# Optimization experiments

Hardware: AMD Instinct MI355X
Metric: run time of the kernel (lower is better)

Reference implementation:

```python
import jax, jax.numpy as jnp
import numpy as np

N_NODES = 50000
N_EDGES = 1600000
CHANNELS = 128
EXPANSION = 50
CUTOFF = 5.0
LOG2 = 0.6931471805599453


def shifted_softplus(x):
    return jax.nn.softplus(x) - LOG2


def gaussian_smearing(r, cutoff=CUTOFF, n=EXPANSION):
    # centers evenly spaced in [0, cutoff]; width set by spacing
    centers = jnp.linspace(0.0, cutoff, n, dtype=r.dtype)
    delta = centers[1] - centers[0]
    coef = 1.0 / (2.0 * delta * delta)
    d = r[:, None] - centers[None, :]          # [E, n]
    return jnp.exp(-coef * d * d)


def setup_inputs() -> dict:
    key = jax.random.key(0)
    ks = jax.random.split(key, 12)
    C, F = CHANNELS, EXPANSION

    def lin(k, fan_in, shape):
        bound = 1.0 / np.sqrt(fan_in)
        return jax.random.uniform(k, shape, jnp.float32, -bound, bound)

    return {
        "features": jax.random.normal(ks[0], (N_NODES, C), jnp.float32),
        "edge_distances": jax.random.uniform(ks[1], (N_EDGES,), jnp.float32) * CUTOFF,
        "W_lin": lin(ks[2], C, (C, C)),
        "Wf1": lin(ks[3], F, (F, C)), "bf1": lin(ks[4], F, (C,)),
        "Wf2": lin(ks[5], C, (C, C)), "bf2": lin(ks[6], C, (C,)),
        "Wm1": lin(ks[7], C, (C, C)), "bm1": lin(ks[8], C, (C,)),
        "Wm2": lin(ks[9], C, (C, C)), "bm2": lin(ks[10], C, (C,)),
        "senders": jax.random.randint(ks[11], (N_EDGES,), 0, N_NODES, jnp.int32),
        "receivers": jax.random.randint(jax.random.fold_in(key, 99), (N_EDGES,), 0, N_NODES, jnp.int32),
    }


def reference(features, edge_distances, W_lin, Wf1, bf1, Wf2, bf2,
              Wm1, bm1, Wm2, bm2, senders, receivers):
    # 1. linear transform of node features (no bias)
    h = features @ W_lin.T                                   # [N, C]
    # 2. learnable radial filter F(r_ij): Gaussian basis -> MLP
    basis = gaussian_smearing(edge_distances)                # [E, F]
    ef = shifted_softplus(basis @ Wf1 + bf1) @ Wf2 + bf2     # [E, C]
    # 3. gather neighbour features, elementwise multiply, scatter-sum
    messages = h[senders] * ef                               # [E, C]
    agg = jax.ops.segment_sum(messages, receivers, num_segments=N_NODES)  # [N, C]
    # 4. output MLP
    return shifted_softplus(agg @ Wm1 + bm1) @ Wm2 + bm2
```

## Files before the change

kernel.cpp:

```cpp
#include <hip/hip_runtime.h>
#include <hip/hip_bf16.h>
#include <math.h>

#define N_NODES 50000
#define N_EDGES 1600000
#define CH 128
#define NF 50
#define NR 8192
#define NB 2048
#define BUCKET_NODES 25
#define CAP 1024
#define PASSA_CHUNK 2048
#define NBLK_SCAT 782
#define NBLK_TB   128
#define NBLK_DH   782

constexpr float DELTA  = 5.0f / 49.0f;
constexpr float COEF   = 1.0f / (2.0f * DELTA * DELTA);
constexpr float LOG2_  = 0.6931471805599453f;
constexpr float RSCALE = (float)(NR - 1) / 5.0f;

typedef short  bf16x8 __attribute__((ext_vector_type(8)));
typedef float  f32x4  __attribute__((ext_vector_type(4)));
typedef unsigned short ushort_t;
typedef unsigned long long u64;

__device__ __forceinline__ float ssp(float x) {
    return fmaxf(x, 0.0f) + __logf(1.0f + __expf(-fabsf(x))) - LOG2_;
}
__device__ __forceinline__ ushort_t f2bf(float x) {
    __hip_bfloat16 b = __float2bfloat16(x);
    return *reinterpret_cast<ushort_t*>(&b);
}
__device__ __forceinline__ float bf2f(ushort_t u) {
    return __uint_as_float(((unsigned)u) << 16);
}
__device__ __forceinline__ float4 f4zero() { return make_float4(0.f, 0.f, 0.f, 0.f); }

__global__ __launch_bounds__(256) void k1_prep(const float* __restrict__ Wlin,
                                               const float* __restrict__ Wm1,
                                               const float* __restrict__ Wm2,
                                               const float* __restrict__ Wf1,
                                               const float* __restrict__ Wf2,
                                               ushort_t* __restrict__ wlhi,
                                               ushort_t* __restrict__ wllo,
                                               ushort_t* __restrict__ wm1hi,
                                               ushort_t* __restrict__ wm1lo,
                                               ushort_t* __restrict__ wm2hi,
                                               ushort_t* __restrict__ wm2lo,
                                               ushort_t* __restrict__ wf1t,
                                               ushort_t* __restrict__ wf2hi,
                                               ushort_t* __restrict__ wf2lo,
                                               int* __restrict__ bcnt) {
    const int tid = threadIdx.x;
    if (blockIdx.x == 64) {
        for (int i = tid; i < NB; i += 256) bcnt[i] = 0;
        return;
    }
    int idx = blockIdx.x * 256 + tid;
    int n = idx >> 7, k = idx & 127;
    {   float w = Wlin[(size_t)n * CH + k];
        ushort_t hi = f2bf(w); wlhi[n * CH + k] = hi; wllo[n * CH + k] = f2bf(w - bf2f(hi)); }
    {   float w = Wm1[(size_t)k * CH + n];
        ushort_t hi = f2bf(w); wm1hi[n * CH + k] = hi; wm1lo[n * CH + k] = f2bf(w - bf2f(hi)); }
    {   float w = Wm2[(size_t)k * CH + n];
        ushort_t hi = f2bf(w); wm2hi[n * CH + k] = hi; wm2lo[n * CH + k] = f2bf(w - bf2f(hi)); }
    if (k < 64) wf1t[n * 64 + k] = (k < NF) ? f2bf(Wf1[k * CH + n]) : (ushort_t)0;
    {   float w = Wf2[(size_t)k * CH + n];
        ushort_t hi = f2bf(w); wf2hi[n * CH + k] = hi; wf2lo[n * CH + k] = f2bf(w - bf2f(hi)); }
}

__device__ void scatter_body(char* smem, int blk,
                             const int* __restrict__ recv,
                             const int* __restrict__ send,
                             const float* __restrict__ dist,
                             int* __restrict__ bcnt,
                             u64* __restrict__ brec) {
    int* bcur   = (int*)smem;
    int* bbaseL = bcur + NB;
    const int tid = threadIdx.x;
    for (int i = tid; i < NB; i += 256) bcur[i] = 0;
    __syncthreads();
    const int e0 = blk * PASSA_CHUNK;
#pragma unroll
    for (int i = 0; i < 8; i++) {
        int e = e0 + tid + i * 256;
        if (e < N_EDGES) atomicAdd(&bcur[recv[e] / BUCKET_NODES], 1);
    }
    __syncthreads();
    for (int i = tid; i < NB; i += 256) {
        int c = bcur[i];
        bbaseL[i] = c ? atomicAdd(&bcnt[i], c) : 0;
        bcur[i] = 0;
    }
    __syncthreads();
#pragma unroll
    for (int i = 0; i < 8; i++) {
        int e = e0 + tid + i * 256;
        if (e < N_EDGES) {
            int r = recv[e];
            int b = r / BUCKET_NODES;
            int rank = bbaseL[b] + atomicAdd(&bcur[b], 1);
            if (rank < CAP) {
                float x = fminf(dist[e] * RSCALE, (float)(NR - 1));
                int ti = __float2int_rn(x);
                u64 rec = (u64)(unsigned)(send[e] | (r << 16)) | ((u64)ti << 32);
                brec[(size_t)b * CAP + rank] = rec;
            }
        }
    }
}

__device__ void table_body(char* smem, int blk,
                           const float* __restrict__ bf1,
                           const float* __restrict__ bf2,
                           const ushort_t* __restrict__ wf1t,
                           const ushort_t* __restrict__ wf2hi,
                           const ushort_t* __restrict__ wf2lo,
                           ushort_t* __restrict__ tabn) {
    ushort_t (*basis)[72] = (ushort_t (*)[72])smem;
    ushort_t (*t1s)[136]  = (ushort_t (*)[136])(smem + 64 * 72 * 2);
    const int tid = threadIdx.x;
    const int g0  = blk * 64;

    for (int i = tid; i < 64 * 64; i += 256) {
        int e = i >> 6, k = i & 63;
        float val = 0.f;
        if (k < NF) {
            float r = (float)(g0 + e) * (5.0f / (float)(NR - 1));
            float d = r - (float)k * DELTA;
            val = __expf(-COEF * d * d);
        }
        basis[e][k] = f2bf(val);
    }
    __syncthreads();

    const int lane = tid & 63;
    const int wv   = tid >> 6;
    const int row  = lane & 15;
    const int quad = lane >> 4;
    const int c0   = (2 * wv) * 16 + row;
    const int c1   = c0 + 16;

    f32x4 acc[2][4];
#pragma unroll
    for (int j = 0; j < 2; j++)
#pragma unroll
        for (int rt = 0; rt < 4; rt++) acc[j][rt] = (f32x4){0.f, 0.f, 0.f, 0.f};

#pragma unroll
    for (int kb = 0; kb < 64; kb += 32) {
        bf16x8 B0 = *(const bf16x8*)&wf1t[c0 * 64 + kb + quad * 8];
        bf16x8 B1 = *(const bf16x8*)&wf1t[c1 * 64 + kb + quad * 8];
#pragma unroll
        for (int rt = 0; rt < 4; rt++) {
            bf16x8 A = *(const bf16x8*)&basis[rt * 16 + row][kb + quad * 8];
            acc[0][rt] = __builtin_amdgcn_mfma_f32_16x16x32_bf16(A, B0, acc[0][rt], 0, 0, 0);
            acc[1][rt] = __builtin_amdgcn_mfma_f32_16x16x32_bf16(A, B1, acc[1][rt], 0, 0, 0);
        }
    }
    {
        float b1v[2] = { bf1[c0], bf1[c1] };
#pragma unroll
        for (int j = 0; j < 2; j++) {
            int c = j ? c1 : c0;
#pragma unroll
            for (int rt = 0; rt < 4; rt++)
#pragma unroll
                for (int rg = 0; rg < 4; rg++) {
                    int e = rt * 16 + quad * 4 + rg;
                    t1s[e][c] = f2bf(ssp(acc[j][rt][rg] + b1v[j]));
                }
        }
    }
    __syncthreads();

#pragma unroll
    for (int j = 0; j < 2; j++)
#pragma unroll
        for (int rt = 0; rt < 4; rt++) acc[j][rt] = (f32x4){0.f, 0.f, 0.f, 0.f};

#pragma unroll
    for (int kb = 0; kb < 128; kb += 32) {
        bf16x8 B0h = *(const bf16x8*)&wf2hi[c0 * CH + kb + quad * 8];
        bf16x8 B0l = *(const bf16x8*)&wf2lo[c0 * CH + kb + quad * 8];
        bf16x8 B1h = *(const bf16x8*)&wf2hi[c1 * CH + kb + quad * 8];
        bf16x8 B1l = *(const bf16x8*)&wf2lo[c1 * CH + kb + quad * 8];
#pragma unroll
        for (int rt = 0; rt < 4; rt++) {
            bf16x8 A = *(const bf16x8*)&t1s[rt * 16 + row][kb + quad * 8];
            acc[0][rt] = __builtin_amdgcn_mfma_f32_16x16x32_bf16(A, B0l, acc[0][rt], 0, 0, 0);
            acc[0][rt] = __builtin_amdgcn_mfma_f32_16x16x32_bf16(A, B0h, acc[0][rt], 0, 0, 0);
            acc[1][rt] = __builtin_amdgcn_mfma_f32_16x16x32_bf16(A, B1l, acc[1][rt], 0, 0, 0);
            acc[1][rt] = __builtin_amdgcn_mfma_f32_16x16x32_bf16(A, B1h, acc[1][rt], 0, 0, 0);
        }
    }
    {
        float b2v[2] = { bf2[c0], bf2[c1] };
#pragma unroll
        for (int j = 0; j < 2; j++) {
            int c = j ? c1 : c0;
#pragma unroll
            for (int rt = 0; rt < 4; rt++)
#pragma unroll
                for (int rg = 0; rg < 4; rg++) {
                    int g = g0 + rt * 16 + quad * 4 + rg;
                    tabn[(size_t)g * CH + c] = f2bf(acc[j][rt][rg] + b2v[j]);
                }
        }
    }
}

__device__ void dense_h_body(char* smem, int blk,
                             const float* __restrict__ X,
                             const ushort_t* __restrict__ Bhi,
                             const ushort_t* __restrict__ Blo,
                             ushort_t* __restrict__ Y) {
    ushort_t (*xs)[136] = (ushort_t (*)[136])smem;
    const int tid  = threadIdx.x;
    const int row0 = blk * 64;

#pragma unroll
    for (int i = 0; i < 8; i++) {
        int idx = tid + i * 256;
        int r   = idx >> 5;
        int c4  = (idx & 31) * 4;
        float4 v = (row0 + r < N_NODES) ? *(const float4*)&X[(size_t)(row0 + r) * CH + c4]
                                        : f4zero();
        ushort4 s;
        s.x = f2bf(v.x); s.y = f2bf(v.y); s.z = f2bf(v.z); s.w = f2bf(v.w);
        *(ushort4*)&xs[r][c4] = s;
    }
    __syncthreads();

    const int lane = tid & 63;
    const int wv   = tid >> 6;
    const int row  = lane & 15;
    const int quad = lane >> 4;
    const int c0   = (2 * wv) * 16 + row;
    const int c1   = c0 + 16;

    f32x4 acc[2][4];
#pragma unroll
    for (int j = 0; j < 2; j++)
#pragma unroll
        for (int rt = 0; rt < 4; rt++) acc[j][rt] = (f32x4){0.f, 0.f, 0.f, 0.f};

#pragma unroll
    for (int kb = 0; kb < 128; kb += 32) {
        bf16x8 B0h = *(const bf16x8*)&Bhi[(size_t)c0 * CH + kb + quad * 8];
        bf16x8 B0l = *(const bf16x8*)&Blo[(size_t)c0 * CH + kb + quad * 8];
        bf16x8 B1h = *(const bf16x8*)&Bhi[(size_t)c1 * CH + kb + quad * 8];
        bf16x8 B1l = *(const bf16x8*)&Blo[(size_t)c1 * CH + kb + quad * 8];
#pragma unroll
        for (int rt = 0; rt < 4; rt++) {
            bf16x8 A = *(const bf16x8*)&xs[rt * 16 + row][kb + quad * 8];
            acc[0][rt] = __builtin_amdgcn_mfma_f32_16x16x32_bf16(A, B0l, acc[0][rt], 0, 0, 0);
            acc[0][rt] = __builtin_amdgcn_mfma_f32_16x16x32_bf16(A, B0h, acc[0][rt], 0, 0, 0);
            acc[1][rt] = __builtin_amdgcn_mfma_f32_16x16x32_bf16(A, B1l, acc[1][rt], 0, 0, 0);
            acc[1][rt] = __builtin_amdgcn_mfma_f32_16x16x32_bf16(A, B1h, acc[1][rt], 0, 0, 0);
        }
    }

#pragma unroll
    for (int j = 0; j < 2; j++) {
        int c = j ? c1 : c0;
#pragma unroll
        for (int rt = 0; rt < 4; rt++)
#pragma unroll
            for (int rg = 0; rg < 4; rg++) {
                int r = row0 + rt * 16 + quad * 4 + rg;
                if (r < N_NODES) Y[(size_t)r * CH + c] = f2bf(acc[j][rt][rg]);
            }
    }
}

__global__ __launch_bounds__(256) void k2_mega(const int* __restrict__ recv,
                                               const int* __restrict__ send,
                                               const float* __restrict__ dist,
                                               int* __restrict__ bcnt,
                                               u64* __restrict__ brec,
                                               const float* __restrict__ bf1,
                                               const float* __restrict__ bf2,
                                               const ushort_t* __restrict__ wf1t,
                                               const ushort_t* __restrict__ wf2hi,
                                               const ushort_t* __restrict__ wf2lo,
                                               ushort_t* __restrict__ tabn,
                                               const float* __restrict__ X,
                                               const ushort_t* __restrict__ wlhi,
                                               const ushort_t* __restrict__ wllo,
                                               ushort_t* __restrict__ h) {
    __shared__ __align__(16) char smem[64 * 72 * 2 + 64 * 136 * 2];
    const int blk = blockIdx.x;
    if (blk < 2 * NBLK_SCAT) {
        if (blk & 1) scatter_body(smem, blk >> 1, recv, send, dist, bcnt, brec);
        else         dense_h_body(smem, blk >> 1, X, wlhi, wllo, h);
    } else {
        table_body(smem, blk - 2 * NBLK_SCAT, bf1, bf2, wf1t, wf2hi, wf2lo, tabn);
    }
}

__global__ __launch_bounds__(256) void sort_gather_mlp(const int* __restrict__ bcnt,
                                                       const u64* __restrict__ brec,
                                                       const ushort_t* __restrict__ h,
                                                       const ushort_t* __restrict__ tabn,
                                                       const ushort_t* __restrict__ B1hi,
                                                       const ushort_t* __restrict__ B1lo,
                                                       const float* __restrict__ bm1,
                                                       const ushort_t* __restrict__ B2hi,
                                                       const ushort_t* __restrict__ B2lo,
                                                       const float* __restrict__ bm2,
                                                       float* __restrict__ OUT) {
    __shared__ int shist[BUCKET_NODES];
    __shared__ int sbeg[BUCKET_NODES];
    __shared__ int sexc[BUCKET_NODES];
    __shared__ unsigned sout[CAP];
    __shared__ __align__(16) ushort_t at[32][136];
    const int b = blockIdx.x, tid = threadIdx.x;
    const int nbase = b * BUCKET_NODES;
    const int nn = min(BUCKET_NODES, N_NODES - nbase);
    if (nn <= 0) return;
    const int m = min(bcnt[b], CAP);
    const u64* my = brec + (size_t)b * CAP;

    for (int i = tid; i < nn; i += 256) shist[i] = 0;
    for (int i = tid; i < 32 * 17; i += 256) {
        bf16x8 z = (bf16x8){0, 0, 0, 0, 0, 0, 0, 0};
        *(bf16x8*)&at[i / 17][(i % 17) * 8] = z;
    }
    __syncthreads();
    for (int i = tid; i < m; i += 256) {
        u64 rec = my[i];
        int l = (int)((rec >> 16) & 0xFFFF) - nbase;
        atomicAdd(&shist[l], 1);
    }
    __syncthreads();
    if (tid == 0) {
        int acc = 0;
#pragma unroll
        for (int l = 0; l < BUCKET_NODES; l++) {
            if (l < nn) { sexc[l] = acc; sbeg[l] = acc; acc += shist[l]; }
        }
    }
    __syncthreads();
    for (int i = tid; i < m; i += 256) {
        u64 rec = my[i];
        int l = (int)((rec >> 16) & 0xFFFF) - nbase;
        int rank = atomicAdd(&sexc[l], 1);
        sout[rank] = (unsigned)(rec & 0xFFFF) | ((unsigned)((rec >> 32) & 0x3FFF) << 16);
    }
    __syncthreads();

    {
        const int g  = tid >> 4;
        const int c8 = (tid & 15) * 8;
        for (int l = g; l < nn; l += 16) {
            const int beg = sbeg[l], end = sbeg[l] + shist[l];
            float acc[8];
#pragma unroll
            for (int j = 0; j < 8; j++) acc[j] = 0.f;

            int e = beg;
            for (; e + 8 <= end; e += 8) {
                unsigned v[8];
#pragma unroll
                for (int u = 0; u < 8; u++) v[u] = sout[e + u];
                bf16x8 hu[8], tn[8];
#pragma unroll
                for (int u = 0; u < 8; u++) {
                    int s  = (int)(v[u] & 0xFFFF);
                    int ti = (int)(v[u] >> 16);
                    hu[u] = *(const bf16x8*)&h[(size_t)s * CH + c8];
                    tn[u] = *(const bf16x8*)&tabn[(size_t)ti * CH + c8];
                }
#pragma unroll
                for (int u = 0; u < 8; u++)
#pragma unroll
                    for (int j = 0; j < 8; j++)
                        acc[j] = fmaf(bf2f((ushort_t)hu[u][j]), bf2f((ushort_t)tn[u][j]), acc[j]);
            }
            for (; e + 4 <= end; e += 4) {
                unsigned v[4];
#pragma unroll
                for (int u = 0; u < 4; u++) v[u] = sout[e + u];
                bf16x8 hu[4], tn[4];
#pragma unroll
                for (int u = 0; u < 4; u++) {
                    int s  = (int)(v[u] & 0xFFFF);
                    int ti = (int)(v[u] >> 16);
                    hu[u] = *(const bf16x8*)&h[(size_t)s * CH + c8];
                    tn[u] = *(const bf16x8*)&tabn[(size_t)ti * CH + c8];
                }
#pragma unroll
                for (int u = 0; u < 4; u++)
#pragma unroll
                    for (int j = 0; j < 8; j++)
                        acc[j] = fmaf(bf2f((ushort_t)hu[u][j]), bf2f((ushort_t)tn[u][j]), acc[j]);
            }
            for (; e < end; e++) {
                unsigned v = sout[e];
                int s  = (int)(v & 0xFFFF);
                int ti = (int)(v >> 16);
                bf16x8 hu = *(const bf16x8*)&h[(size_t)s * CH + c8];
                bf16x8 tn = *(const bf16x8*)&tabn[(size_t)ti * CH + c8];
#pragma unroll
                for (int j = 0; j < 8; j++)
                    acc[j] = fmaf(bf2f((ushort_t)hu[j]), bf2f((ushort_t)tn[j]), acc[j]);
            }

            bf16x8 o;
#pragma unroll
            for (int j = 0; j < 8; j++) o[j] = (short)f2bf(acc[j]);
            *(bf16x8*)&at[l][c8] = o;
        }
    }
    __syncthreads();

    const int lane = tid & 63;
    const int wv   = tid >> 6;
    const int row  = lane & 15;
    const int quad = lane >> 4;
    const int c0   = (2 * wv) * 16 + row;
    const int c1   = c0 + 16;

    f32x4 acc[2][2];
#pragma unroll
    for (int j = 0; j < 2; j++)
#pragma unroll
        for (int rt = 0; rt < 2; rt++) acc[j][rt] = (f32x4){0.f, 0.f, 0.f, 0.f};

#pragma unroll
    for (int kb = 0; kb < 128; kb += 32) {
        bf16x8 B0h = *(const bf16x8*)&B1hi[(size_t)c0 * CH + kb + quad * 8];
        bf16x8 B0l = *(const bf16x8*)&B1lo[(size_t)c0 * CH + kb + quad * 8];
        bf16x8 B1h_ = *(const bf16x8*)&B1hi[(size_t)c1 * CH + kb + quad * 8];
        bf16x8 B1l_ = *(const bf16x8*)&B1lo[(size_t)c1 * CH + kb + quad * 8];
#pragma unroll
        for (int rt = 0; rt < 2; rt++) {
            bf16x8 A = *(const bf16x8*)&at[rt * 16 + row][kb + quad * 8];
            acc[0][rt] = __builtin_amdgcn_mfma_f32_16x16x32_bf16(A, B0l, acc[0][rt], 0, 0, 0);
            acc[0][rt] = __builtin_amdgcn_mfma_f32_16x16x32_bf16(A, B0h, acc[0][rt], 0, 0, 0);
            acc[1][rt] = __builtin_amdgcn_mfma_f32_16x16x32_bf16(A, B1l_, acc[1][rt], 0, 0, 0);
            acc[1][rt] = __builtin_amdgcn_mfma_f32_16x16x32_bf16(A, B1h_, acc[1][rt], 0, 0, 0);
        }
    }
    __syncthreads();
    {
        float bv[2] = { bm1[c0], bm1[c1] };
#pragma unroll
        for (int j = 0; j < 2; j++) {
            int c = j ? c1 : c0;
#pragma unroll
            for (int rt = 0; rt < 2; rt++)
#pragma unroll
                for (int rg = 0; rg < 4; rg++)
                    at[rt * 16 + quad * 4 + rg][c] = f2bf(ssp(acc[j][rt][rg] + bv[j]));
        }
    }
    __syncthreads();

#pragma unroll
    for (int j = 0; j < 2; j++)
#pragma unroll
        for (int rt = 0; rt < 2; rt++) acc[j][rt] = (f32x4){0.f, 0.f, 0.f, 0.f};

#pragma unroll
    for (int kb = 0; kb < 128; kb += 32) {
        bf16x8 B0h = *(const bf16x8*)&B2hi[(size_t)c0 * CH + kb + quad * 8];
        bf16x8 B0l = *(const bf16x8*)&B2lo[(size_t)c0 * CH + kb + quad * 8];
        bf16x8 B1h_ = *(const bf16x8*)&B2hi[(size_t)c1 * CH + kb + quad * 8];
        bf16x8 B1l_ = *(const bf16x8*)&B2lo[(size_t)c1 * CH + kb + quad * 8];
#pragma unroll
        for (int rt = 0; rt < 2; rt++) {
            bf16x8 A = *(const bf16x8*)&at[rt * 16 + row][kb + quad * 8];
            acc[0][rt] = __builtin_amdgcn_mfma_f32_16x16x32_bf16(A, B0l, acc[0][rt], 0, 0, 0);
            acc[0][rt] = __builtin_amdgcn_mfma_f32_16x16x32_bf16(A, B0h, acc[0][rt], 0, 0, 0);
            acc[1][rt] = __builtin_amdgcn_mfma_f32_16x16x32_bf16(A, B1l_, acc[1][rt], 0, 0, 0);
            acc[1][rt] = __builtin_amdgcn_mfma_f32_16x16x32_bf16(A, B1h_, acc[1][rt], 0, 0, 0);
        }
    }
    {
        float bv[2] = { bm2[c0], bm2[c1] };
#pragma unroll
        for (int j = 0; j < 2; j++) {
            int c = j ? c1 : c0;
#pragma unroll
            for (int rt = 0; rt < 2; rt++)
#pragma unroll
                for (int rg = 0; rg < 4; rg++) {
                    int r = rt * 16 + quad * 4 + rg;
                    if (r < nn) OUT[(size_t)(nbase + r) * CH + c] = acc[j][rt][rg] + bv[j];
                }
        }
    }
}

extern "C" void kernel_launch(void* const* d_in, const int* in_sizes, int n_in,
                              void* d_out, int out_size, void* d_ws, size_t ws_size,
                              hipStream_t stream) {
    const float* features = (const float*)d_in[0];
    const float* dist     = (const float*)d_in[1];
    const float* W_lin    = (const float*)d_in[2];
    const float* Wf1      = (const float*)d_in[3];
    const float* bf1      = (const float*)d_in[4];
    const float* Wf2      = (const float*)d_in[5];
    const float* bf2      = (const float*)d_in[6];
    const float* Wm1      = (const float*)d_in[7];
    const float* bm1      = (const float*)d_in[8];
    const float* Wm2      = (const float*)d_in[9];
    const float* bm2      = (const float*)d_in[10];
    const int* senders    = (const int*)d_in[11];
    const int* receivers  = (const int*)d_in[12];
    float* out = (float*)d_out;

    u64* brec       = (u64*)d_ws;
    ushort_t* h     = (ushort_t*)(brec + (size_t)NB * CAP);
    ushort_t* tabn  = h + (size_t)N_NODES * CH;
    int* bcnt       = (int*)(tabn + (size_t)NR * CH);
    ushort_t* wlhi  = (ushort_t*)(bcnt + NB);
    ushort_t* wllo  = wlhi  + CH * CH;
    ushort_t* wm1hi = wllo  + CH * CH;
    ushort_t* wm1lo = wm1hi + CH * CH;
    ushort_t* wm2hi = wm1lo + CH * CH;
    ushort_t* wm2lo = wm2hi + CH * CH;
    ushort_t* wf1t  = wm2lo + CH * CH;
    ushort_t* wf2hi = wf1t  + CH * 64;
    ushort_t* wf2lo = wf2hi + CH * CH;

    k1_prep<<<65, 256, 0, stream>>>(W_lin, Wm1, Wm2, Wf1, Wf2,
                                    wlhi, wllo, wm1hi, wm1lo, wm2hi, wm2lo,
                                    wf1t, wf2hi, wf2lo, bcnt);

    k2_mega<<<2 * NBLK_SCAT + NBLK_TB, 256, 0, stream>>>(
        receivers, senders, dist, bcnt, brec,
        bf1, bf2, wf1t, wf2hi, wf2lo, tabn,
        features, wlhi, wllo, h);

    sort_gather_mlp<<<NB, 256, 0, stream>>>(bcnt, brec, h, tabn,
                                            wm1hi, wm1lo, bm1,
                                            wm2hi, wm2lo, bm2, out);
}
```

Measured before the change: 271.0 us.

## Use 32-node buckets, batch scatter loads, and reorder mega-kernel block roles

Bucket size goes from 25 to 32 nodes, which gives fewer buckets (1563) and a larger per-bucket capacity of 1280. The sort/gather/MLP blocks then fill a full 32-row MFMA tile with no padding rows. The scatter pass now loads all receiver, sender and distance values up front in register arrays on full chunks, so memory latency overlaps before the LDS atomics. Block roles in the fused kernel are reordered so scatter blocks are scheduled first, then table, then dense-h, instead of interleaving scatter and dense-h. Larger buckets raise per-block work in the final kernel and change overflow risk against the capacity limit.

```diff
diff --git a/kernel.cpp b/kernel.cpp
--- a/kernel.cpp
+++ b/kernel.cpp
@@ -7,9 +7,9 @@
 #define CH 128
 #define NF 50
 #define NR 8192
-#define NB 2048
-#define BUCKET_NODES 25
-#define CAP 1024
+#define NB 1563
+#define BUCKET_NODES 32
+#define CAP 1280
 #define PASSA_CHUNK 2048
 #define NBLK_SCAT 782
 #define NBLK_TB   128
@@ -82,10 +82,20 @@
     for (int i = tid; i < NB; i += 256) bcur[i] = 0;
     __syncthreads();
     const int e0 = blk * PASSA_CHUNK;
-#pragma unroll
-    for (int i = 0; i < 8; i++) {
-        int e = e0 + tid + i * 256;
-        if (e < N_EDGES) atomicAdd(&bcur[recv[e] / BUCKET_NODES], 1);
+    const bool full = (e0 + PASSA_CHUNK <= N_EDGES);
+    int r8[8];
+    if (full) {
+#pragma unroll
+        for (int i = 0; i < 8; i++) r8[i] = recv[e0 + tid + i * 256];
+#pragma unroll
+        for (int i = 0; i < 8; i++) atomicAdd(&bcur[r8[i] / BUCKET_NODES], 1);
+    } else {
+#pragma unroll
+        for (int i = 0; i < 8; i++) {
+            int e = e0 + tid + i * 256;
+            r8[i] = (e < N_EDGES) ? recv[e] : -1;
+            if (r8[i] >= 0) atomicAdd(&bcur[r8[i] / BUCKET_NODES], 1);
+        }
     }
     __syncthreads();
     for (int i = tid; i < NB; i += 256) {
@@ -94,18 +104,37 @@
         bcur[i] = 0;
     }
     __syncthreads();
-#pragma unroll
-    for (int i = 0; i < 8; i++) {
-        int e = e0 + tid + i * 256;
-        if (e < N_EDGES) {
-            int r = recv[e];
-            int b = r / BUCKET_NODES;
+    if (full) {
+        int s8[8]; float d8[8];
+#pragma unroll
+        for (int i = 0; i < 8; i++) {
+            int e = e0 + tid + i * 256;
+            s8[i] = send[e];
+            d8[i] = dist[e];
+        }
+#pragma unroll
+        for (int i = 0; i < 8; i++) {
+            int b = r8[i] / BUCKET_NODES;
             int rank = bbaseL[b] + atomicAdd(&bcur[b], 1);
             if (rank < CAP) {
-                float x = fminf(dist[e] * RSCALE, (float)(NR - 1));
-                int ti = __float2int_rn(x);
-                u64 rec = (u64)(unsigned)(send[e] | (r << 16)) | ((u64)ti << 32);
+                int ti = __float2int_rn(fminf(d8[i] * RSCALE, (float)(NR - 1)));
+                u64 rec = (u64)(unsigned)(s8[i] | (r8[i] << 16)) | ((u64)ti << 32);
                 brec[(size_t)b * CAP + rank] = rec;
+            }
+        }
+    } else {
+#pragma unroll
+        for (int i = 0; i < 8; i++) {
+            int e = e0 + tid + i * 256;
+            if (e < N_EDGES) {
+                int r = r8[i];
+                int b = r / BUCKET_NODES;
+                int rank = bbaseL[b] + atomicAdd(&bcur[b], 1);
+                if (rank < CAP) {
+                    int ti = __float2int_rn(fminf(dist[e] * RSCALE, (float)(NR - 1)));
+                    u64 rec = (u64)(unsigned)(send[e] | (r << 16)) | ((u64)ti << 32);
+                    brec[(size_t)b * CAP + rank] = rec;
+                }
             }
         }
     }
@@ -292,11 +321,12 @@
                                                ushort_t* __restrict__ h) {
     __shared__ __align__(16) char smem[64 * 72 * 2 + 64 * 136 * 2];
     const int blk = blockIdx.x;
-    if (blk < 2 * NBLK_SCAT) {
-        if (blk & 1) scatter_body(smem, blk >> 1, recv, send, dist, bcnt, brec);
-        else         dense_h_body(smem, blk >> 1, X, wlhi, wllo, h);
+    if (blk < NBLK_SCAT) {
+        scatter_body(smem, blk, recv, send, dist, bcnt, brec);
+    } else if (blk < NBLK_SCAT + NBLK_TB) {
+        table_body(smem, blk - NBLK_SCAT, bf1, bf2, wf1t, wf2hi, wf2lo, tabn);
     } else {
-        table_body(smem, blk - 2 * NBLK_SCAT, bf1, bf2, wf1t, wf2hi, wf2lo, tabn);
+        dense_h_body(smem, blk - NBLK_SCAT - NBLK_TB, X, wlhi, wllo, h);
     }
 }
 
@@ -323,7 +353,7 @@
     const int m = min(bcnt[b], CAP);
     const u64* my = brec + (size_t)b * CAP;
 
-    for (int i = tid; i < nn; i += 256) shist[i] = 0;
+    if (tid < BUCKET_NODES) shist[tid] = 0;
     for (int i = tid; i < 32 * 17; i += 256) {
         bf16x8 z = (bf16x8){0, 0, 0, 0, 0, 0, 0, 0};
         *(bf16x8*)&at[i / 17][(i % 17) * 8] = z;
@@ -531,7 +561,7 @@
                                     wlhi, wllo, wm1hi, wm1lo, wm2hi, wm2lo,
                                     wf1t, wf2hi, wf2lo, bcnt);
 
-    k2_mega<<<2 * NBLK_SCAT + NBLK_TB, 256, 0, stream>>>(
+    k2_mega<<<NBLK_SCAT + NBLK_TB + NBLK_DH, 256, 0, stream>>>(
         receivers, senders, dist, bcnt, brec,
         bf1, bf2, wf1t, wf2hi, wf2lo, tabn,
         features, wlhi, wllo, h);
```

After: 258.8 us. 4.5% less time.
